# Performance work log

Hardware: AMD Instinct MI355X
Metric: run time of the kernel (lower is better)

Reference implementation:

```python
import jax, jax.numpy as jnp
import numpy as np

N, M, D = 4096, 8192, 512

def setup_inputs() -> dict:
    key = jax.random.key(0)
    k1, k2, k3, k4 = jax.random.split(key, 4)
    X = jax.random.normal(k1, (N, D), dtype=jnp.float32)
    SV = jax.random.normal(k2, (M, D), dtype=jnp.float32)
    DC = jax.random.normal(k3, (1, M), dtype=jnp.float32)
    IC = jax.random.normal(k4, (1,), dtype=jnp.float32)
    gamma = jnp.float32(1.0 / D)
    return {"X": X, "SV": SV, "DC": DC, "IC": IC, "gamma": gamma}

def reference(X, SV, DC, IC, gamma):
    # Squared pairwise L2 distances via GEMM expansion (same math as
    # ||SV - x||^2 without materializing the [N, M, D] broadcast tensor):
    # d2[n, m] = ||x_n||^2 + ||sv_m||^2 - 2 * x_n . sv_m
    x2 = jnp.sum(X * X, axis=1)          # [N]
    sv2 = jnp.sum(SV * SV, axis=1)       # [M]
    cross = jnp.einsum("nd,md->nm", X, SV)  # [N, M]
    d2 = jnp.maximum(x2[:, None] + sv2[None, :] - 2.0 * cross, 0.0)
    k = jnp.exp(-gamma * d2)             # RBF kernel values [N, M]
    # Weighted reduction over support vectors + intercept -> decision values [N]
    return jnp.sum(k * DC, axis=1) + IC
```

## Files before the change

kernel.cpp:

```cpp
#include <hip/hip_runtime.h>
#include <stdint.h>

#define NN 4096
#define MM 8192
#define DD 512

typedef __bf16 bf16x8 __attribute__((ext_vector_type(8)));
typedef float f32x4 __attribute__((ext_vector_type(4)));
typedef float f32x16 __attribute__((ext_vector_type(16)));

template <int CTRL>
__device__ __forceinline__ float dpp_radd(float x) {
  int xi = __float_as_int(x);
  int mv = __builtin_amdgcn_update_dpp(xi, xi, CTRL, 0xF, 0xF, false);
  return x + __int_as_float(mv);
}
__device__ __forceinline__ float swz_add_xor16(float x) {
  int sv = __builtin_amdgcn_ds_swizzle(__float_as_int(x), 0x401F);
  return x + __int_as_float(sv);
}

__global__ __launch_bounds__(256) void convert_norm_kernel(
    const float* __restrict__ X, const float* __restrict__ SV,
    bf16x8* __restrict__ Xf, bf16x8* __restrict__ SVf,
    float* __restrict__ x2, float* __restrict__ sv2,
    float* __restrict__ out, const float* __restrict__ IC) {
  int wid = blockIdx.x * 4 + (threadIdx.x >> 6);
  int lane = threadIdx.x & 63;
  const float* src;
  float* nrm;
  bf16x8* dstF;
  bool isX = (wid < NN);
  int r = isX ? wid : wid - NN;
  if (isX) {
    src = X + (size_t)r * DD;
    nrm = x2 + r;
    dstF = Xf;
    if (lane == 0) out[r] = IC[0];
  } else {
    src = SV + (size_t)r * DD;
    nrm = sv2 + r;
    dstF = SVf;
  }
  const f32x4* s = (const f32x4*)src;
  f32x4 a = s[2 * lane];
  f32x4 b = s[2 * lane + 1];
  float sum = a.x * a.x + a.y * a.y + a.z * a.z + a.w * a.w +
              b.x * b.x + b.y * b.y + b.z * b.z + b.w * b.w;
  bf16x8 o;
  o[0] = (__bf16)a.x; o[1] = (__bf16)a.y; o[2] = (__bf16)a.z; o[3] = (__bf16)a.w;
  o[4] = (__bf16)b.x; o[5] = (__bf16)b.y; o[6] = (__bf16)b.z; o[7] = (__bf16)b.w;
  dstF[((size_t)((r >> 5) * 32 + (lane >> 1))) * 64 + (lane & 1) * 32 + (r & 31)] = o;
#pragma unroll
  for (int m = 32; m >= 1; m >>= 1) sum += __shfl_xor(sum, m, 64);
  if (lane == 0) *nrm = sum;
}

__global__ __launch_bounds__(256, 3) void rbf_gemm_kernel(
    const bf16x8* __restrict__ Xf, const bf16x8* __restrict__ SVf,
    const float* __restrict__ x2, const float* __restrict__ sv2,
    const float* __restrict__ DC, const float* __restrict__ gamma_p,
    float* __restrict__ out) {
  const int t = threadIdx.x;
  const int lane = t & 63;
  const int wave = t >> 6;
  const int n0 = blockIdx.x * 128;
  const int m0 = blockIdx.y * 128;

  const int wave_m = wave & 1;
  const int wave_n = wave >> 1;
  const int l31 = lane & 31;
  const int lhi = lane >> 5;

  const int rgA = blockIdx.x * 4 + wave_n * 2;
  const int rgB = blockIdx.y * 4 + wave_m * 2;
  const bf16x8* ap0 = Xf + (size_t)rgA * 2048 + lane;
  const bf16x8* ap1 = ap0 + 2048;
  const bf16x8* bp0 = SVf + (size_t)rgB * 2048 + lane;
  const bf16x8* bp1 = bp0 + 2048;

  f32x16 acc[2][2];
#pragma unroll
  for (int i = 0; i < 2; ++i)
#pragma unroll
    for (int j = 0; j < 2; ++j)
#pragma unroll
      for (int r = 0; r < 16; ++r) acc[i][j][r] = 0.0f;

  bf16x8 a0 = ap0[0], a1 = ap1[0], b0 = bp0[0], b1 = bp1[0];
#pragma unroll
  for (int sg = 0; sg < 32; ++sg) {
    bf16x8 na0, na1, nb0, nb1;
    if (sg + 1 < 32) {
      const size_t o = (size_t)(sg + 1) * 64;
      na0 = ap0[o];
      na1 = ap1[o];
      nb0 = bp0[o];
      nb1 = bp1[o];
    }
    acc[0][0] = __builtin_amdgcn_mfma_f32_32x32x16_bf16(a0, b0, acc[0][0], 0, 0, 0);
    acc[0][1] = __builtin_amdgcn_mfma_f32_32x32x16_bf16(a0, b1, acc[0][1], 0, 0, 0);
    acc[1][0] = __builtin_amdgcn_mfma_f32_32x32x16_bf16(a1, b0, acc[1][0], 0, 0, 0);
    acc[1][1] = __builtin_amdgcn_mfma_f32_32x32x16_bf16(a1, b1, acc[1][1], 0, 0, 0);
    a0 = na0; a1 = na1; b0 = nb0; b1 = nb1;
  }

  const float g = gamma_p[0];
  const float c2 = g * 1.4426950408889634f;

  float sv2v[2], dcv[2];
  const int colb = m0 + wave_m * 64 + l31;
  sv2v[0] = sv2[colb];
  dcv[0] = DC[colb];
  sv2v[1] = sv2[colb + 32];
  dcv[1] = DC[colb + 32];

#pragma unroll
  for (int i = 0; i < 2; ++i) {
    const int rowb = n0 + wave_n * 64 + i * 32 + 4 * lhi;
    float val[16];
#pragma unroll
    for (int g4 = 0; g4 < 4; ++g4) {
      f32x4 xv = *(const f32x4*)(x2 + rowb + 8 * g4);
#pragma unroll
      for (int r2 = 0; r2 < 4; ++r2) {
        const int reg = g4 * 4 + r2;
        float v = 0.0f;
#pragma unroll
        for (int j = 0; j < 2; ++j) {
          float d2 = xv[r2] + sv2v[j] - 2.0f * acc[i][j][reg];
          d2 = fmaxf(d2, 0.0f);
          v += exp2f(-c2 * d2) * dcv[j];
        }
        val[reg] = v;
      }
    }
#pragma unroll
    for (int reg = 0; reg < 16; ++reg) {
      float v = val[reg];
      v = dpp_radd<0x121>(v);
      v = dpp_radd<0x122>(v);
      v = dpp_radd<0x124>(v);
      v = dpp_radd<0x128>(v);
      val[reg] = swz_add_xor16(v);
    }
    if (l31 == 0) {
#pragma unroll
      for (int g4 = 0; g4 < 4; ++g4)
#pragma unroll
        for (int r2 = 0; r2 < 4; ++r2)
          atomicAdd(&out[rowb + 8 * g4 + r2], val[g4 * 4 + r2]);
    }
  }
}

extern "C" void kernel_launch(void* const* d_in, const int* in_sizes, int n_in,
                              void* d_out, int out_size, void* d_ws, size_t ws_size,
                              hipStream_t stream) {
  const float* X = (const float*)d_in[0];
  const float* SV = (const float*)d_in[1];
  const float* DC = (const float*)d_in[2];
  const float* IC = (const float*)d_in[3];
  const float* gamma = (const float*)d_in[4];
  float* out = (float*)d_out;

  char* ws = (char*)d_ws;
  bf16x8* Xf = (bf16x8*)ws;
  bf16x8* SVf = (bf16x8*)(ws + (size_t)NN * DD * 2);
  float* x2 = (float*)(ws + (size_t)(NN + MM) * DD * 2);
  float* sv2 = x2 + NN;

  convert_norm_kernel<<<(NN + MM) / 4, 256, 0, stream>>>(X, SV, Xf, SVf, x2, sv2, out, IC);
  dim3 grid(NN / 128, MM / 128);
  rbf_gemm_kernel<<<grid, 256, 0, stream>>>(Xf, SVf, x2, sv2, DC, gamma, out);
}
```

Measured before the change: 150.1 us.

## Stage SV tile in LDS and stream X through 512-thread blocks

The GEMM kernel now loads a 64-column SV tile into LDS once per block using global_load_lds and reuses it across 1024 X rows in two passes of 8 waves. Before, each block fetched both operands from global memory for a 128x128 tile. The convert kernel now handles 32 rows per block and goes through an LDS transpose so that its global stores are coalesced. In exchange, A operands are loaded without explicit prefetching, which may expose latency, and the grid has fewer, larger blocks with higher LDS use.

```diff
diff --git a/kernel.cpp b/kernel.cpp
--- a/kernel.cpp
+++ b/kernel.cpp
@@ -8,6 +8,12 @@
 typedef __bf16 bf16x8 __attribute__((ext_vector_type(8)));
 typedef float f32x4 __attribute__((ext_vector_type(4)));
 typedef float f32x16 __attribute__((ext_vector_type(16)));
+
+__device__ __forceinline__ void load_lds16(const void* g, void* l) {
+  __builtin_amdgcn_global_load_lds(
+      (const __attribute__((address_space(1))) unsigned int*)g,
+      (__attribute__((address_space(3))) unsigned int*)l, 16, 0, 0);
+}
 
 template <int CTRL>
 __device__ __forceinline__ float dpp_radd(float x) {
@@ -25,131 +31,136 @@
     bf16x8* __restrict__ Xf, bf16x8* __restrict__ SVf,
     float* __restrict__ x2, float* __restrict__ sv2,
     float* __restrict__ out, const float* __restrict__ IC) {
-  int wid = blockIdx.x * 4 + (threadIdx.x >> 6);
-  int lane = threadIdx.x & 63;
-  const float* src;
-  float* nrm;
-  bf16x8* dstF;
-  bool isX = (wid < NN);
-  int r = isX ? wid : wid - NN;
-  if (isX) {
-    src = X + (size_t)r * DD;
-    nrm = x2 + r;
-    dstF = Xf;
-    if (lane == 0) out[r] = IC[0];
-  } else {
-    src = SV + (size_t)r * DD;
-    nrm = sv2 + r;
-    dstF = SVf;
+  __shared__ bf16x8 L[2048];
+  const int g = blockIdx.x;
+  const bool isX = g < (NN / 32);
+  const int rg = isX ? g : g - (NN / 32);
+  const float* src = (isX ? X : SV) + (size_t)rg * 32 * DD;
+  bf16x8* dstF = (isX ? Xf : SVf) + (size_t)rg * 2048;
+  float* nrm = (isX ? x2 : sv2) + rg * 32;
+  const int t = threadIdx.x;
+  const int lane = t & 63, wv = t >> 6;
+
+  if (isX && t < 32) out[rg * 32 + t] = IC[0];
+
+#pragma unroll
+  for (int i = 0; i < 8; ++i) {
+    const int r = wv * 8 + i;
+    const f32x4* s = (const f32x4*)(src + (size_t)r * DD);
+    f32x4 a = s[2 * lane];
+    f32x4 b = s[2 * lane + 1];
+    float sum = a.x * a.x + a.y * a.y + a.z * a.z + a.w * a.w +
+                b.x * b.x + b.y * b.y + b.z * b.z + b.w * b.w;
+    bf16x8 o;
+    o[0] = (__bf16)a.x; o[1] = (__bf16)a.y; o[2] = (__bf16)a.z; o[3] = (__bf16)a.w;
+    o[4] = (__bf16)b.x; o[5] = (__bf16)b.y; o[6] = (__bf16)b.z; o[7] = (__bf16)b.w;
+    L[r * 64 + ((lane + r) & 63)] = o;
+#pragma unroll
+    for (int m = 32; m >= 1; m >>= 1) sum += __shfl_xor(sum, m, 64);
+    if (lane == 0) nrm[r] = sum;
   }
-  const f32x4* s = (const f32x4*)src;
-  f32x4 a = s[2 * lane];
-  f32x4 b = s[2 * lane + 1];
-  float sum = a.x * a.x + a.y * a.y + a.z * a.z + a.w * a.w +
-              b.x * b.x + b.y * b.y + b.z * b.z + b.w * b.w;
-  bf16x8 o;
-  o[0] = (__bf16)a.x; o[1] = (__bf16)a.y; o[2] = (__bf16)a.z; o[3] = (__bf16)a.w;
-  o[4] = (__bf16)b.x; o[5] = (__bf16)b.y; o[6] = (__bf16)b.z; o[7] = (__bf16)b.w;
-  dstF[((size_t)((r >> 5) * 32 + (lane >> 1))) * 64 + (lane & 1) * 32 + (r & 31)] = o;
+  __syncthreads();
 #pragma unroll
-  for (int m = 32; m >= 1; m >>= 1) sum += __shfl_xor(sum, m, 64);
-  if (lane == 0) *nrm = sum;
+  for (int it = 0; it < 8; ++it) {
+    const int c = it * 256 + t;
+    const int sg = c >> 6, h = (c >> 5) & 1, r31 = c & 31;
+    dstF[c] = L[r31 * 64 + ((sg * 2 + h + r31) & 63)];
+  }
 }
 
-__global__ __launch_bounds__(256, 3) void rbf_gemm_kernel(
+__global__ __launch_bounds__(512, 4) void rbf_gemm_kernel(
     const bf16x8* __restrict__ Xf, const bf16x8* __restrict__ SVf,
     const float* __restrict__ x2, const float* __restrict__ sv2,
     const float* __restrict__ DC, const float* __restrict__ gamma_p,
     float* __restrict__ out) {
+  __shared__ bf16x8 Bs[4096];
+
   const int t = threadIdx.x;
   const int lane = t & 63;
   const int wave = t >> 6;
-  const int n0 = blockIdx.x * 128;
-  const int m0 = blockIdx.y * 128;
-
-  const int wave_m = wave & 1;
-  const int wave_n = wave >> 1;
+  const int cm = blockIdx.x;
+  const int nq = blockIdx.y;
+  const int m0 = cm * 64;
   const int l31 = lane & 31;
   const int lhi = lane >> 5;
 
-  const int rgA = blockIdx.x * 4 + wave_n * 2;
-  const int rgB = blockIdx.y * 4 + wave_m * 2;
-  const bf16x8* ap0 = Xf + (size_t)rgA * 2048 + lane;
-  const bf16x8* ap1 = ap0 + 2048;
-  const bf16x8* bp0 = SVf + (size_t)rgB * 2048 + lane;
-  const bf16x8* bp1 = bp0 + 2048;
-
-  f32x16 acc[2][2];
+  const bf16x8* bsrc = SVf + (size_t)cm * 4096;
 #pragma unroll
-  for (int i = 0; i < 2; ++i)
-#pragma unroll
-    for (int j = 0; j < 2; ++j)
-#pragma unroll
-      for (int r = 0; r < 16; ++r) acc[i][j][r] = 0.0f;
-
-  bf16x8 a0 = ap0[0], a1 = ap1[0], b0 = bp0[0], b1 = bp1[0];
-#pragma unroll
-  for (int sg = 0; sg < 32; ++sg) {
-    bf16x8 na0, na1, nb0, nb1;
-    if (sg + 1 < 32) {
-      const size_t o = (size_t)(sg + 1) * 64;
-      na0 = ap0[o];
-      na1 = ap1[o];
-      nb0 = bp0[o];
-      nb1 = bp1[o];
-    }
-    acc[0][0] = __builtin_amdgcn_mfma_f32_32x32x16_bf16(a0, b0, acc[0][0], 0, 0, 0);
-    acc[0][1] = __builtin_amdgcn_mfma_f32_32x32x16_bf16(a0, b1, acc[0][1], 0, 0, 0);
-    acc[1][0] = __builtin_amdgcn_mfma_f32_32x32x16_bf16(a1, b0, acc[1][0], 0, 0, 0);
-    acc[1][1] = __builtin_amdgcn_mfma_f32_32x32x16_bf16(a1, b1, acc[1][1], 0, 0, 0);
-    a0 = na0; a1 = na1; b0 = nb0; b1 = nb1;
+  for (int it = 0; it < 8; ++it) {
+    const int c = it * 512 + t;
+    load_lds16(bsrc + c, &Bs[c]);
   }
+  __syncthreads();
 
   const float g = gamma_p[0];
   const float c2 = g * 1.4426950408889634f;
+  float sv2v[2], dcv[2];
+  sv2v[0] = sv2[m0 + l31];
+  dcv[0] = DC[m0 + l31];
+  sv2v[1] = sv2[m0 + 32 + l31];
+  dcv[1] = DC[m0 + 32 + l31];
 
-  float sv2v[2], dcv[2];
-  const int colb = m0 + wave_m * 64 + l31;
-  sv2v[0] = sv2[colb];
-  dcv[0] = DC[colb];
-  sv2v[1] = sv2[colb + 32];
-  dcv[1] = DC[colb + 32];
+  for (int pass = 0; pass < 2; ++pass) {
+    const int nb = nq * 1024 + pass * 512 + wave * 64;
+    const bf16x8* ap0 = Xf + (size_t)(nb >> 5) * 2048 + lane;
+    const bf16x8* ap1 = ap0 + 2048;
+
+    f32x16 acc[2][2];
+#pragma unroll
+    for (int i = 0; i < 2; ++i)
+#pragma unroll
+      for (int j = 0; j < 2; ++j)
+#pragma unroll
+        for (int r = 0; r < 16; ++r) acc[i][j][r] = 0.0f;
 
 #pragma unroll
-  for (int i = 0; i < 2; ++i) {
-    const int rowb = n0 + wave_n * 64 + i * 32 + 4 * lhi;
-    float val[16];
+    for (int sg = 0; sg < 32; ++sg) {
+      bf16x8 a0 = ap0[(size_t)sg * 64];
+      bf16x8 a1 = ap1[(size_t)sg * 64];
+      bf16x8 b0 = Bs[sg * 64 + lane];
+      bf16x8 b1 = Bs[2048 + sg * 64 + lane];
+      acc[0][0] = __builtin_amdgcn_mfma_f32_32x32x16_bf16(a0, b0, acc[0][0], 0, 0, 0);
+      acc[0][1] = __builtin_amdgcn_mfma_f32_32x32x16_bf16(a0, b1, acc[0][1], 0, 0, 0);
+      acc[1][0] = __builtin_amdgcn_mfma_f32_32x32x16_bf16(a1, b0, acc[1][0], 0, 0, 0);
+      acc[1][1] = __builtin_amdgcn_mfma_f32_32x32x16_bf16(a1, b1, acc[1][1], 0, 0, 0);
+    }
+
 #pragma unroll
-    for (int g4 = 0; g4 < 4; ++g4) {
-      f32x4 xv = *(const f32x4*)(x2 + rowb + 8 * g4);
+    for (int i = 0; i < 2; ++i) {
+      const int rowb = nb + i * 32 + 4 * lhi;
+      float val[16];
 #pragma unroll
-      for (int r2 = 0; r2 < 4; ++r2) {
-        const int reg = g4 * 4 + r2;
-        float v = 0.0f;
+      for (int g4 = 0; g4 < 4; ++g4) {
+        f32x4 xv = *(const f32x4*)(x2 + rowb + 8 * g4);
 #pragma unroll
-        for (int j = 0; j < 2; ++j) {
-          float d2 = xv[r2] + sv2v[j] - 2.0f * acc[i][j][reg];
-          d2 = fmaxf(d2, 0.0f);
-          v += exp2f(-c2 * d2) * dcv[j];
+        for (int r2 = 0; r2 < 4; ++r2) {
+          const int reg = g4 * 4 + r2;
+          float v = 0.0f;
+#pragma unroll
+          for (int j = 0; j < 2; ++j) {
+            float d2 = xv[r2] + sv2v[j] - 2.0f * acc[i][j][reg];
+            d2 = fmaxf(d2, 0.0f);
+            v += exp2f(-c2 * d2) * dcv[j];
+          }
+          val[reg] = v;
         }
-        val[reg] = v;
       }
-    }
 #pragma unroll
-    for (int reg = 0; reg < 16; ++reg) {
-      float v = val[reg];
-      v = dpp_radd<0x121>(v);
-      v = dpp_radd<0x122>(v);
-      v = dpp_radd<0x124>(v);
-      v = dpp_radd<0x128>(v);
-      val[reg] = swz_add_xor16(v);
-    }
-    if (l31 == 0) {
+      for (int reg = 0; reg < 16; ++reg) {
+        float v = val[reg];
+        v = dpp_radd<0x121>(v);
+        v = dpp_radd<0x122>(v);
+        v = dpp_radd<0x124>(v);
+        v = dpp_radd<0x128>(v);
+        val[reg] = swz_add_xor16(v);
+      }
+      if (l31 == 0) {
 #pragma unroll
-      for (int g4 = 0; g4 < 4; ++g4)
+        for (int g4 = 0; g4 < 4; ++g4)
 #pragma unroll
-        for (int r2 = 0; r2 < 4; ++r2)
-          atomicAdd(&out[rowb + 8 * g4 + r2], val[g4 * 4 + r2]);
+          for (int r2 = 0; r2 < 4; ++r2)
+            atomicAdd(&out[rowb + 8 * g4 + r2], val[g4 * 4 + r2]);
+      }
     }
   }
 }
@@ -170,7 +181,7 @@
   float* x2 = (float*)(ws + (size_t)(NN + MM) * DD * 2);
   float* sv2 = x2 + NN;
 
-  convert_norm_kernel<<<(NN + MM) / 4, 256, 0, stream>>>(X, SV, Xf, SVf, x2, sv2, out, IC);
-  dim3 grid(NN / 128, MM / 128);
-  rbf_gemm_kernel<<<grid, 256, 0, stream>>>(Xf, SVf, x2, sv2, DC, gamma, out);
+  convert_norm_kernel<<<(NN + MM) / 32, 256, 0, stream>>>(X, SV, Xf, SVf, x2, sv2, out, IC);
+  dim3 grid(MM / 64, NN / 1024);
+  rbf_gemm_kernel<<<grid, 512, 0, stream>>>(Xf, SVf, x2, sv2, DC, gamma, out);
 }
```

New measurement: 285.2 us. 1.9x slower.
